# Kernel tuning notes

Measured on AMD Instinct MI355X. Metric: run time of the kernel, lower is better.

## Reference

```python
import jax, jax.numpy as jnp
import numpy as np

B, C, H, W, K, NH = 4, 128, 64, 64, 7, 8
DH = C // NH          # per-head dim
PAD = (K - 1) // 2    # symmetric padding since K is odd


def setup_inputs() -> dict:
    key = jax.random.key(0)
    ks = jax.random.split(key, 9)
    s = 1.0 / np.sqrt(C)
    f32 = jnp.float32
    return {
        "x": jax.random.normal(ks[0], (B, C, H, W), f32),
        "wq": jax.random.normal(ks[1], (C, C), f32) * s,
        "bq": jax.random.normal(ks[2], (C,), f32) * 0.01,
        "wk": jax.random.normal(ks[3], (C, C), f32) * s,
        "bk": jax.random.normal(ks[4], (C,), f32) * 0.01,
        "wv": jax.random.normal(ks[5], (C, C), f32) * s,
        "bv": jax.random.normal(ks[6], (C,), f32) * 0.01,
        "pos_h": jax.random.normal(ks[7], (NH, K), f32) * 0.02,
        "pos_w": jax.random.normal(ks[8], (NH, K), f32) * 0.02,
    }


def _unfold(p):
    # p: [B,C,H+K-1,W+K-1] -> [B,C,H,W,K,K] (KxK neighborhood per pixel),
    # matching torch .unfold(2,K,1).unfold(3,K,1). Loop is over fixed kernel size only.
    p1 = jnp.stack([p[:, :, i:i + H, :] for i in range(K)], axis=-1)      # [B,C,H,W+K-1,K]
    return jnp.stack([p1[:, :, :, j:j + W, :] for j in range(K)], axis=-1)  # [B,C,H,W,K,K]


def reference(x, wq, bq, wk, bk, wv, bv, pos_h, pos_w):
    cx = x  # cx defaults to x in the original module
    pc = jnp.pad(cx, ((0, 0), (0, 0), (PAD, PAD), (PAD, PAD)))
    # 1x1 convs are pointwise channel mixes
    k = jnp.einsum('oc,bchw->bohw', wk, pc) + bk[None, :, None, None]
    v = jnp.einsum('oc,bchw->bohw', wv, pc) + bv[None, :, None, None]
    q = jnp.einsum('oc,bchw->bohw', wq, x) + bq[None, :, None, None]

    ku = _unfold(k).reshape(B, NH, DH, H, W, K, K)
    vu = _unfold(v).reshape(B, NH, DH, H, W, K, K)
    qh = q.reshape(B, NH, DH, H, W)

    # per-pixel logits over KxK neighborhood
    logits = jnp.einsum('bndhw,bndhwij->bnhwij', qh, ku)  # [B,NH,H,W,K,K]
    logits = logits + pos_h[None, :, None, None, :, None] + pos_w[None, :, None, None, None, :]

    weights = jax.nn.softmax(logits.reshape(B, NH, H, W, K * K), axis=-1)
    out = jnp.einsum('bnhwk,bndhwk->bndhw', weights, vu.reshape(B, NH, DH, H, W, K * K))
    return out.reshape(B, C, H, W)
```

## Files before the change

kernel.cpp:

```cpp
#include <hip/hip_runtime.h>
#include <cmath>

constexpr int Bn = 4, Cn = 128, Hn = 64, Wn = 64, Kn = 7, NHn = 8, DHn = 16, PADn = 3;
constexpr int HWn = Hn * Wn;
constexpr int TS = 16;
constexpr int HALO = TS + Kn - 1;
constexpr int NPIX = HALO * HALO;
constexpr int PSTRIDE_U16 = 24;
constexpr int PSTRIDE_U32 = 12;

typedef float f32x4 __attribute__((ext_vector_type(4)));
typedef short short8 __attribute__((ext_vector_type(8)));
typedef unsigned int u32x4 __attribute__((ext_vector_type(4)));
typedef unsigned short u16x4 __attribute__((ext_vector_type(4)));
typedef unsigned short u16x8 __attribute__((ext_vector_type(8)));

__device__ __forceinline__ unsigned short f32_to_bf16_rne(float f) {
  unsigned u = __float_as_uint(f);
  unsigned r = u + 0x7fffu + ((u >> 16) & 1u);
  return (unsigned short)(r >> 16);
}
__device__ __forceinline__ float bf16_to_f32(unsigned short h) {
  return __uint_as_float(((unsigned)h) << 16);
}
__device__ __forceinline__ float bflo(unsigned u) { return __uint_as_float(u << 16); }
__device__ __forceinline__ float bfhi(unsigned u) { return __uint_as_float(u & 0xffff0000u); }

__global__ __launch_bounds__(256)
void prep(const float* __restrict__ x,
          const float* __restrict__ wq, const float* __restrict__ wk,
          const float* __restrict__ wv,
          unsigned short* __restrict__ Whl, unsigned short* __restrict__ xThl)
{
  const int t = threadIdx.x;
  if (blockIdx.z == 4) {
    if (blockIdx.y != 0 || blockIdx.x >= 48) return;
    const int mat = blockIdx.x >> 4;
    const int chunk = blockIdx.x & 15;
    const float* W = (mat == 0) ? wq : (mat == 1) ? wk : wv;
    const int i = (chunk * 256 + t) * 4;
    const f32x4 v = *reinterpret_cast<const f32x4*>(W + i);
    unsigned short h[4], l[4];
#pragma unroll
    for (int j = 0; j < 4; ++j) {
      h[j] = f32_to_bf16_rne(v[j]);
      l[j] = f32_to_bf16_rne(v[j] - bf16_to_f32(h[j]));
    }
    unsigned short* base = Whl + (size_t)mat * 2 * 16384;
    *reinterpret_cast<uint2*>(base + i) =
        make_uint2(h[0] | ((unsigned)h[1] << 16), h[2] | ((unsigned)h[3] << 16));
    *reinterpret_cast<uint2*>(base + 16384 + i) =
        make_uint2(l[0] | ((unsigned)l[1] << 16), l[2] | ((unsigned)l[3] << 16));
    return;
  }

  __shared__ float sm[32][65];
  const int b   = blockIdx.z;
  const int c0g = blockIdx.y * 32;
  const int p0g = blockIdx.x * 64;
  const float* xb = x + (size_t)b * Cn * HWn;

#pragma unroll
  for (int rep = 0; rep < 2; ++rep) {
    const int cl = rep * 16 + (t >> 4);
    const int pl = (t & 15) * 4;
    const f32x4 v = *reinterpret_cast<const f32x4*>(xb + (size_t)(c0g + cl) * HWn + p0g + pl);
    sm[cl][pl + 0] = v[0]; sm[cl][pl + 1] = v[1];
    sm[cl][pl + 2] = v[2]; sm[cl][pl + 3] = v[3];
  }
  __syncthreads();

  const int pl = t >> 2;
  const int c0 = (t & 3) * 8;
  u32x4 hw, lw;
#pragma unroll
  for (int j = 0; j < 4; ++j) {
    const float v0 = sm[c0 + 2 * j][pl];
    const float v1 = sm[c0 + 2 * j + 1][pl];
    const unsigned short h0 = f32_to_bf16_rne(v0);
    const unsigned short h1 = f32_to_bf16_rne(v1);
    const unsigned short l0 = f32_to_bf16_rne(v0 - bf16_to_f32(h0));
    const unsigned short l1 = f32_to_bf16_rne(v1 - bf16_to_f32(h1));
    hw[j] = h0 | ((unsigned)h1 << 16);
    lw[j] = l0 | ((unsigned)l1 << 16);
  }
  unsigned short* dst = xThl + (size_t)b * 2 * HWn * Cn + (size_t)(p0g + pl) * Cn + c0g + c0;
  *reinterpret_cast<u32x4*>(dst)            = hw;
  *reinterpret_cast<u32x4*>(dst + HWn * Cn) = lw;
}

__global__ __launch_bounds__(64)
void qkv_mfma(const unsigned short* __restrict__ Whl,
              const unsigned short* __restrict__ xThl,
              const float* __restrict__ bq_, const float* __restrict__ bk_,
              const float* __restrict__ bv_,
              float* __restrict__ qo, unsigned short* __restrict__ kbf,
              unsigned short* __restrict__ vbf)
{
  const int z   = blockIdx.z;
  const int mat = z >> 2;
  const int b   = z & 3;
  const float* bias = (mat == 0) ? bq_ : (mat == 1) ? bk_ : bv_;

  const int lane = threadIdx.x;
  const int r    = lane & 15;
  const int quad = lane >> 4;
  const int mbase = blockIdx.y * 64;
  const int nbase = blockIdx.x * 64;

  const unsigned short* Wm = Whl  + (size_t)mat * 2 * Cn * Cn;
  const unsigned short* Xb = xThl + (size_t)b   * 2 * HWn * Cn;

  f32x4 acc[4][4] = {};

#pragma unroll
  for (int ks = 0; ks < 4; ++ks) {
    const int kk = ks * 32 + quad * 8;
    short8 Ah[4], Al[4], Bh[4], Bl[4];
#pragma unroll
    for (int mt = 0; mt < 4; ++mt) {
      const unsigned short* p = Wm + (size_t)(mbase + mt * 16 + r) * Cn + kk;
      Ah[mt] = *reinterpret_cast<const short8*>(p);
      Al[mt] = *reinterpret_cast<const short8*>(p + Cn * Cn);
    }
#pragma unroll
    for (int nt = 0; nt < 4; ++nt) {
      const unsigned short* p = Xb + (size_t)(nbase + nt * 16 + r) * Cn + kk;
      Bh[nt] = *reinterpret_cast<const short8*>(p);
      Bl[nt] = *reinterpret_cast<const short8*>(p + HWn * Cn);
    }
#pragma unroll
    for (int mt = 0; mt < 4; ++mt)
#pragma unroll
      for (int nt = 0; nt < 4; ++nt) {
        acc[mt][nt] = __builtin_amdgcn_mfma_f32_16x16x32_bf16(Ah[mt], Bh[nt], acc[mt][nt], 0, 0, 0);
        acc[mt][nt] = __builtin_amdgcn_mfma_f32_16x16x32_bf16(Ah[mt], Bl[nt], acc[mt][nt], 0, 0, 0);
        acc[mt][nt] = __builtin_amdgcn_mfma_f32_16x16x32_bf16(Al[mt], Bh[nt], acc[mt][nt], 0, 0, 0);
      }
  }

#pragma unroll
  for (int mt = 0; mt < 4; ++mt) {
    const int n = blockIdx.y * 4 + mt;
    const f32x4 b4 = *reinterpret_cast<const f32x4*>(bias + mbase + mt * 16 + quad * 4);
#pragma unroll
    for (int nt = 0; nt < 4; ++nt) {
      const int p = nbase + nt * 16 + r;
      const size_t off = ((size_t)((b * NHn + n) * HWn + p)) * DHn + quad * 4;
      f32x4 val = acc[mt][nt] + b4;
      if (mat == 0) {
        *reinterpret_cast<f32x4*>(qo + off) = val;
      } else {
        unsigned short* y = (mat == 1) ? kbf : vbf;
        u16x4 pk;
        pk[0] = f32_to_bf16_rne(val[0]); pk[1] = f32_to_bf16_rne(val[1]);
        pk[2] = f32_to_bf16_rne(val[2]); pk[3] = f32_to_bf16_rne(val[3]);
        *reinterpret_cast<u16x4*>(y + off) = pk;
      }
    }
  }
}

__global__ __launch_bounds__(256)
void sasa_attn(const float* __restrict__ q, const unsigned short* __restrict__ kbf,
               const unsigned short* __restrict__ vbf, const float* __restrict__ bk_,
               const float* __restrict__ bv_, const float* __restrict__ pos_h,
               const float* __restrict__ pos_w, float* __restrict__ out)
{
  __shared__ __align__(16) unsigned short ksm[NPIX * PSTRIDE_U16];
  __shared__ __align__(16) unsigned short vsm[NPIX * PSTRIDE_U16];

  const int z  = blockIdx.z;
  const int b  = z >> 3;
  const int n  = z & 7;
  const int h0 = blockIdx.y * TS;
  const int w0 = blockIdx.x * TS;
  const int tid = threadIdx.x;
  const int tx = tid & 15;
  const int ty = tid >> 4;
  const int cbase = n * DHn;

  const unsigned short* kb = kbf + ((size_t)(b * NHn + n) * HWn) * DHn;
  const unsigned short* vb = vbf + ((size_t)(b * NHn + n) * HWn) * DHn;

  u16x8 kb0, kb1, vb0, vb1;
#pragma unroll
  for (int j = 0; j < 8; ++j) {
    kb0[j] = f32_to_bf16_rne(bk_[cbase + j]);
    kb1[j] = f32_to_bf16_rne(bk_[cbase + 8 + j]);
    vb0[j] = f32_to_bf16_rne(bv_[cbase + j]);
    vb1[j] = f32_to_bf16_rne(bv_[cbase + 8 + j]);
  }

  for (int c = tid; c < NPIX * 2; c += 256) {
    const int pix  = c >> 1;
    const int half = c & 1;
    const int hh = pix / HALO;
    const int ww = pix - hh * HALO;
    const int gh = h0 + hh - PADn;
    const int gw = w0 + ww - PADn;
    const bool inb = (gh >= 0) && (gh < Hn) && (gw >= 0) && (gw < Wn);
    u16x8 kd, vd;
    if (inb) {
      const size_t src = ((size_t)(gh * Wn + gw)) * DHn + half * 8;
      kd = *reinterpret_cast<const u16x8*>(kb + src);
      vd = *reinterpret_cast<const u16x8*>(vb + src);
    } else {
      kd = half ? kb1 : kb0;
      vd = half ? vb1 : vb0;
    }
    const int dst = pix * PSTRIDE_U16 + half * 8;
    *reinterpret_cast<u16x8*>(ksm + dst) = kd;
    *reinterpret_cast<u16x8*>(vsm + dst) = vd;
  }

  const int h = h0 + ty, w = w0 + tx;
  const int p = h * Wn + w;
  const float* qp = q + ((size_t)(b * NHn + n) * HWn + p) * DHn;
  float qr[DHn];
#pragma unroll
  for (int j = 0; j < 4; ++j) {
    const f32x4 t4 = *reinterpret_cast<const f32x4*>(qp + j * 4);
    qr[j * 4 + 0] = t4[0]; qr[j * 4 + 1] = t4[1];
    qr[j * 4 + 2] = t4[2]; qr[j * 4 + 3] = t4[3];
  }

  __syncthreads();

  const unsigned* ksu = reinterpret_cast<const unsigned*>(ksm);
  const unsigned* vsu = reinterpret_cast<const unsigned*>(vsm);

  float logits[Kn * Kn];
#pragma unroll
  for (int i = 0; i < Kn; ++i) {
    const float ph = pos_h[n * Kn + i];
#pragma unroll
    for (int j = 0; j < Kn; ++j) {
      const int base = ((ty + i) * HALO + (tx + j)) * PSTRIDE_U32;
      const u32x4 a = *reinterpret_cast<const u32x4*>(ksu + base);
      const u32x4 c = *reinterpret_cast<const u32x4*>(ksu + base + 4);
      float acc = qr[0] * bflo(a[0]);
      acc = fmaf(qr[1],  bfhi(a[0]), acc);
      acc = fmaf(qr[2],  bflo(a[1]), acc);  acc = fmaf(qr[3],  bfhi(a[1]), acc);
      acc = fmaf(qr[4],  bflo(a[2]), acc);  acc = fmaf(qr[5],  bfhi(a[2]), acc);
      acc = fmaf(qr[6],  bflo(a[3]), acc);  acc = fmaf(qr[7],  bfhi(a[3]), acc);
      acc = fmaf(qr[8],  bflo(c[0]), acc);  acc = fmaf(qr[9],  bfhi(c[0]), acc);
      acc = fmaf(qr[10], bflo(c[1]), acc);  acc = fmaf(qr[11], bfhi(c[1]), acc);
      acc = fmaf(qr[12], bflo(c[2]), acc);  acc = fmaf(qr[13], bfhi(c[2]), acc);
      acc = fmaf(qr[14], bflo(c[3]), acc);  acc = fmaf(qr[15], bfhi(c[3]), acc);
      logits[i * Kn + j] = acc + ph + pos_w[n * Kn + j];
    }
  }

  float mx = -1e30f;
#pragma unroll
  for (int t = 0; t < Kn * Kn; ++t) mx = fmaxf(mx, logits[t]);
  float sum = 0.0f;
#pragma unroll
  for (int t = 0; t < Kn * Kn; ++t) {
    const float e = __expf(logits[t] - mx);
    logits[t] = e;
    sum += e;
  }
  const float inv = 1.0f / sum;

  float o[DHn] = {};
#pragma unroll
  for (int i = 0; i < Kn; ++i) {
#pragma unroll
    for (int j = 0; j < Kn; ++j) {
      const float wt = logits[i * Kn + j];
      const int base = ((ty + i) * HALO + (tx + j)) * PSTRIDE_U32;
      const u32x4 a = *reinterpret_cast<const u32x4*>(vsu + base);
      const u32x4 c = *reinterpret_cast<const u32x4*>(vsu + base + 4);
      o[0]  = fmaf(wt, bflo(a[0]), o[0]);   o[1]  = fmaf(wt, bfhi(a[0]), o[1]);
      o[2]  = fmaf(wt, bflo(a[1]), o[2]);   o[3]  = fmaf(wt, bfhi(a[1]), o[3]);
      o[4]  = fmaf(wt, bflo(a[2]), o[4]);   o[5]  = fmaf(wt, bfhi(a[2]), o[5]);
      o[6]  = fmaf(wt, bflo(a[3]), o[6]);   o[7]  = fmaf(wt, bfhi(a[3]), o[7]);
      o[8]  = fmaf(wt, bflo(c[0]), o[8]);   o[9]  = fmaf(wt, bfhi(c[0]), o[9]);
      o[10] = fmaf(wt, bflo(c[1]), o[10]);  o[11] = fmaf(wt, bfhi(c[1]), o[11]);
      o[12] = fmaf(wt, bflo(c[2]), o[12]);  o[13] = fmaf(wt, bfhi(c[2]), o[13]);
      o[14] = fmaf(wt, bflo(c[3]), o[14]);  o[15] = fmaf(wt, bfhi(c[3]), o[15]);
    }
  }

  float* ob = out + ((size_t)(b * Cn + cbase)) * HWn + p;
#pragma unroll
  for (int d = 0; d < DHn; ++d) ob[(size_t)d * HWn] = o[d] * inv;
}

extern "C" void kernel_launch(void* const* d_in, const int* in_sizes, int n_in,
                              void* d_out, int out_size, void* d_ws, size_t ws_size,
                              hipStream_t stream) {
  const float* x     = (const float*)d_in[0];
  const float* wq    = (const float*)d_in[1];
  const float* bq    = (const float*)d_in[2];
  const float* wk    = (const float*)d_in[3];
  const float* bk    = (const float*)d_in[4];
  const float* wv    = (const float*)d_in[5];
  const float* bv    = (const float*)d_in[6];
  const float* pos_h = (const float*)d_in[7];
  const float* pos_w = (const float*)d_in[8];
  float* out = (float*)d_out;

  const size_t tensor_elems = (size_t)Bn * Cn * HWn;
  float*          q    = (float*)d_ws;
  unsigned short* kbf  = (unsigned short*)(q + tensor_elems);
  unsigned short* vbf  = kbf + tensor_elems;
  unsigned short* Whl  = vbf + tensor_elems;
  unsigned short* xThl = Whl + (size_t)3 * 2 * Cn * Cn;

  dim3 gp(HWn / 64, Cn / 32, Bn + 1);
  prep<<<gp, 256, 0, stream>>>(x, wq, wk, wv, Whl, xThl);

  dim3 g1(HWn / 64, Cn / 64, 3 * Bn);
  qkv_mfma<<<g1, 64, 0, stream>>>(Whl, xThl, bq, bk, bv, q, kbf, vbf);

  dim3 g2(Wn / TS, Hn / TS, Bn * NHn);
  sasa_attn<<<g2, 256, 0, stream>>>(q, kbf, vbf, bk, bv, pos_h, pos_w, out);
}
```

Before: 110.8 us.

## Split head dimension across two threads per pixel in SASA attention kernel

Each pixel is now handled by two lanes, each owning half of the 16-element head dimension, so the block grows from 256 to 512 threads. The partial q·k dot products are combined with a lane shuffle, which halves per-thread register use for q, logits and the output accumulators. This is meant to raise occupancy and parallelism in the attention stage. The cost is redundant softmax work in both lanes, an extra shuffle per logit, and output stores that are now strided across lanes.

```diff
diff --git a/kernel.cpp b/kernel.cpp
--- a/kernel.cpp
+++ b/kernel.cpp
@@ -161,7 +161,7 @@
   }
 }
 
-__global__ __launch_bounds__(256)
+__global__ __launch_bounds__(512)
 void sasa_attn(const float* __restrict__ q, const unsigned short* __restrict__ kbf,
                const unsigned short* __restrict__ vbf, const float* __restrict__ bk_,
                const float* __restrict__ bv_, const float* __restrict__ pos_h,
@@ -176,8 +176,11 @@
   const int h0 = blockIdx.y * TS;
   const int w0 = blockIdx.x * TS;
   const int tid = threadIdx.x;
-  const int tx = tid & 15;
-  const int ty = tid >> 4;
+  const int pix   = tid >> 1;
+  const int dhalf = tid & 1;
+  const int d0    = dhalf * 8;
+  const int tx = pix & 15;
+  const int ty = pix >> 4;
   const int cbase = n * DHn;
 
   const unsigned short* kb = kbf + ((size_t)(b * NHn + n) * HWn) * DHn;
@@ -192,11 +195,11 @@
     vb1[j] = f32_to_bf16_rne(bv_[cbase + 8 + j]);
   }
 
-  for (int c = tid; c < NPIX * 2; c += 256) {
-    const int pix  = c >> 1;
+  for (int c = tid; c < NPIX * 2; c += 512) {
+    const int hp   = c >> 1;
     const int half = c & 1;
-    const int hh = pix / HALO;
-    const int ww = pix - hh * HALO;
+    const int hh = hp / HALO;
+    const int ww = hp - hh * HALO;
     const int gh = h0 + hh - PADn;
     const int gw = w0 + ww - PADn;
     const bool inb = (gh >= 0) && (gh < Hn) && (gw >= 0) && (gw < Wn);
@@ -209,20 +212,20 @@
       kd = half ? kb1 : kb0;
       vd = half ? vb1 : vb0;
     }
-    const int dst = pix * PSTRIDE_U16 + half * 8;
+    const int dst = hp * PSTRIDE_U16 + half * 8;
     *reinterpret_cast<u16x8*>(ksm + dst) = kd;
     *reinterpret_cast<u16x8*>(vsm + dst) = vd;
   }
 
   const int h = h0 + ty, w = w0 + tx;
   const int p = h * Wn + w;
-  const float* qp = q + ((size_t)(b * NHn + n) * HWn + p) * DHn;
-  float qr[DHn];
-#pragma unroll
-  for (int j = 0; j < 4; ++j) {
-    const f32x4 t4 = *reinterpret_cast<const f32x4*>(qp + j * 4);
-    qr[j * 4 + 0] = t4[0]; qr[j * 4 + 1] = t4[1];
-    qr[j * 4 + 2] = t4[2]; qr[j * 4 + 3] = t4[3];
+  const float* qp = q + ((size_t)(b * NHn + n) * HWn + p) * DHn + d0;
+  float qr[8];
+  {
+    const f32x4 t0 = *reinterpret_cast<const f32x4*>(qp);
+    const f32x4 t1 = *reinterpret_cast<const f32x4*>(qp + 4);
+    qr[0] = t0[0]; qr[1] = t0[1]; qr[2] = t0[2]; qr[3] = t0[3];
+    qr[4] = t1[0]; qr[5] = t1[1]; qr[6] = t1[2]; qr[7] = t1[3];
   }
 
   __syncthreads();
@@ -236,18 +239,14 @@
     const float ph = pos_h[n * Kn + i];
 #pragma unroll
     for (int j = 0; j < Kn; ++j) {
-      const int base = ((ty + i) * HALO + (tx + j)) * PSTRIDE_U32;
+      const int base = ((ty + i) * HALO + (tx + j)) * PSTRIDE_U32 + dhalf * 4;
       const u32x4 a = *reinterpret_cast<const u32x4*>(ksu + base);
-      const u32x4 c = *reinterpret_cast<const u32x4*>(ksu + base + 4);
       float acc = qr[0] * bflo(a[0]);
-      acc = fmaf(qr[1],  bfhi(a[0]), acc);
-      acc = fmaf(qr[2],  bflo(a[1]), acc);  acc = fmaf(qr[3],  bfhi(a[1]), acc);
-      acc = fmaf(qr[4],  bflo(a[2]), acc);  acc = fmaf(qr[5],  bfhi(a[2]), acc);
-      acc = fmaf(qr[6],  bflo(a[3]), acc);  acc = fmaf(qr[7],  bfhi(a[3]), acc);
-      acc = fmaf(qr[8],  bflo(c[0]), acc);  acc = fmaf(qr[9],  bfhi(c[0]), acc);
-      acc = fmaf(qr[10], bflo(c[1]), acc);  acc = fmaf(qr[11], bfhi(c[1]), acc);
-      acc = fmaf(qr[12], bflo(c[2]), acc);  acc = fmaf(qr[13], bfhi(c[2]), acc);
-      acc = fmaf(qr[14], bflo(c[3]), acc);  acc = fmaf(qr[15], bfhi(c[3]), acc);
+      acc = fmaf(qr[1], bfhi(a[0]), acc);
+      acc = fmaf(qr[2], bflo(a[1]), acc);  acc = fmaf(qr[3], bfhi(a[1]), acc);
+      acc = fmaf(qr[4], bflo(a[2]), acc);  acc = fmaf(qr[5], bfhi(a[2]), acc);
+      acc = fmaf(qr[6], bflo(a[3]), acc);  acc = fmaf(qr[7], bfhi(a[3]), acc);
+      acc += __shfl_xor(acc, 1);
       logits[i * Kn + j] = acc + ph + pos_w[n * Kn + j];
     }
   }
@@ -264,29 +263,24 @@
   }
   const float inv = 1.0f / sum;
 
-  float o[DHn] = {};
+  float o[8] = {};
 #pragma unroll
   for (int i = 0; i < Kn; ++i) {
 #pragma unroll
     for (int j = 0; j < Kn; ++j) {
       const float wt = logits[i * Kn + j];
-      const int base = ((ty + i) * HALO + (tx + j)) * PSTRIDE_U32;
+      const int base = ((ty + i) * HALO + (tx + j)) * PSTRIDE_U32 + dhalf * 4;
       const u32x4 a = *reinterpret_cast<const u32x4*>(vsu + base);
-      const u32x4 c = *reinterpret_cast<const u32x4*>(vsu + base + 4);
-      o[0]  = fmaf(wt, bflo(a[0]), o[0]);   o[1]  = fmaf(wt, bfhi(a[0]), o[1]);
-      o[2]  = fmaf(wt, bflo(a[1]), o[2]);   o[3]  = fmaf(wt, bfhi(a[1]), o[3]);
-      o[4]  = fmaf(wt, bflo(a[2]), o[4]);   o[5]  = fmaf(wt, bfhi(a[2]), o[5]);
-      o[6]  = fmaf(wt, bflo(a[3]), o[6]);   o[7]  = fmaf(wt, bfhi(a[3]), o[7]);
-      o[8]  = fmaf(wt, bflo(c[0]), o[8]);   o[9]  = fmaf(wt, bfhi(c[0]), o[9]);
-      o[10] = fmaf(wt, bflo(c[1]), o[10]);  o[11] = fmaf(wt, bfhi(c[1]), o[11]);
-      o[12] = fmaf(wt, bflo(c[2]), o[12]);  o[13] = fmaf(wt, bfhi(c[2]), o[13]);
-      o[14] = fmaf(wt, bflo(c[3]), o[14]);  o[15] = fmaf(wt, bfhi(c[3]), o[15]);
-    }
-  }
-
-  float* ob = out + ((size_t)(b * Cn + cbase)) * HWn + p;
-#pragma unroll
-  for (int d = 0; d < DHn; ++d) ob[(size_t)d * HWn] = o[d] * inv;
+      o[0] = fmaf(wt, bflo(a[0]), o[0]);  o[1] = fmaf(wt, bfhi(a[0]), o[1]);
+      o[2] = fmaf(wt, bflo(a[1]), o[2]);  o[3] = fmaf(wt, bfhi(a[1]), o[3]);
+      o[4] = fmaf(wt, bflo(a[2]), o[4]);  o[5] = fmaf(wt, bfhi(a[2]), o[5]);
+      o[6] = fmaf(wt, bflo(a[3]), o[6]);  o[7] = fmaf(wt, bfhi(a[3]), o[7]);
+    }
+  }
+
+  float* ob = out + ((size_t)(b * Cn + cbase + d0)) * HWn + p;
+#pragma unroll
+  for (int d = 0; d < 8; ++d) ob[(size_t)d * HWn] = o[d] * inv;
 }
 
 extern "C" void kernel_launch(void* const* d_in, const int* in_sizes, int n_in,
@@ -317,5 +311,5 @@
   qkv_mfma<<<g1, 64, 0, stream>>>(Whl, xThl, bq, bk, bv, q, kbf, vbf);
 
   dim3 g2(Wn / TS, Hn / TS, Bn * NHn);
-  sasa_attn<<<g2, 256, 0, stream>>>(q, kbf, vbf, bk, bv, pos_h, pos_w, out);
-}
+  sasa_attn<<<g2, 512, 0, stream>>>(q, kbf, vbf, bk, bv, pos_h, pos_w, out);
+}
```

Result: slower. 113.3 us (+2.3%).
